# Performance work log

Hardware: AMD Instinct MI355X
Metric: run time of the kernel (lower is better)

The kernel has to match this reference:

```python
import math
import jax, jax.numpy as jnp
import numpy as np

L = 4        # number of base-MLP layers
B = 16       # batch of weight-space samples
N = 256      # base-MLP width (n_in = n_out = N)
C_IN = 16    # input channels per weight entry
C_OUT = 16   # output channels per weight entry
HID = 64     # siren hidden dim
W0 = 1.0
W0_FIRST = 30.0
FINAL_NORM = math.sqrt((2 * L + 7) * C_IN)


def setup_inputs() -> dict:
    key = jax.random.key(0)
    ks = jax.random.split(key, 17)
    d = {}
    for i in range(L):
        d[f"w{i}"] = jax.random.normal(ks[i], (B, N, N, C_IN), jnp.float32) * 0.02
        d[f"b{i}"] = jax.random.normal(ks[L + i], (B, N, C_IN), jnp.float32) * 0.02
    def u(k, shape, scale):
        return jax.random.uniform(k, shape, jnp.float32, -scale, scale)
    # SIREN-style init scales
    d["s_w0"] = u(ks[8], (3, HID), 1.0 / 3.0)
    d["s_b0"] = u(ks[9], (HID,), 1.0 / math.sqrt(3.0))
    d["s_w1"] = u(ks[10], (HID, HID), math.sqrt(6.0 / HID) / W0)
    d["s_b1"] = u(ks[11], (HID,), 1.0 / math.sqrt(HID))
    d["s_w2"] = u(ks[12], (HID, HID), math.sqrt(6.0 / HID) / W0)
    d["s_b2"] = u(ks[13], (HID,), 1.0 / math.sqrt(HID))
    d["s_wo"] = u(ks[14], (HID, C_IN * C_OUT), math.sqrt(6.0 / HID) / W0)
    d["s_bo"] = u(ks[15], (C_IN * C_OUT,), 1.0 / math.sqrt(HID))
    return d


def _siren(x, sp):
    sw0, sb0, sw1, sb1, sw2, sb2, swo, sbo = sp
    h = jnp.sin(W0_FIRST * (x @ sw0 + sb0))
    h = jnp.sin(W0 * (h @ sw1 + sb1))
    h = jnp.sin(W0 * (h @ sw2 + sb2))
    return (h @ swo + sbo) / FINAL_NORM


def _forward(ws, bs, sp):
    term_idx = jnp.linspace(-1.0, 1.0, num=14)
    layer_idx = jnp.linspace(-1.0, 1.0, num=L)
    grid = jnp.stack(jnp.meshgrid(layer_idx, layer_idx, indexing='ij'), axis=-1)  # (L,L,2)

    g_in = jnp.concatenate([jnp.broadcast_to(grid, (4, L, L, 2)),
                            jnp.broadcast_to(term_idx[:4, None, None, None], (4, L, L, 1))], -1)
    global_terms = _siren(g_in, sp).reshape(4, L, L, C_IN, C_OUT)

    dgrid = jnp.transpose(jnp.diagonal(grid))          # (L,2)
    d_in = jnp.concatenate([jnp.broadcast_to(dgrid, (6, L, 2)),
                            jnp.broadcast_to(term_idx[4:10, None, None], (6, L, 1))], -1)
    diag_terms = _siren(d_in, sp).reshape(6, L, C_IN, C_OUT)

    p1 = jnp.transpose(jnp.diagonal(grid, offset=1))   # (L-1,2)
    p1_in = jnp.concatenate([jnp.broadcast_to(p1, (2, L - 1, 2)),
                             jnp.broadcast_to(term_idx[10:12, None, None], (2, L - 1, 1))], -1)
    diag_p1 = _siren(p1_in, sp).reshape(2, L - 1, C_IN, C_OUT)

    m1 = jnp.transpose(jnp.diagonal(grid, offset=-1))  # (L-1,2)
    m1_in = jnp.concatenate([jnp.broadcast_to(m1, (2, L - 1, 2)),
                             jnp.broadcast_to(term_idx[12:14, None, None], (2, L - 1, 1))], -1)
    diag_m1 = _siren(m1_in, sp).reshape(2, L - 1, C_IN, C_OUT)

    t_w_otherw, t_w_otherb = global_terms[0], global_terms[1]
    t_b_otherw, t_b_otherb = global_terms[2], global_terms[3]
    t_w_wrow, t_w_wcol, t_w_w = diag_terms[0], diag_terms[1], diag_terms[2]
    t_w_b, t_b_wcol, t_bb = diag_terms[3], diag_terms[4], diag_terms[5]
    t_w_wm1, t_w_bm1 = diag_m1[0], diag_m1[1]
    t_w_wp1, t_b_wp1 = diag_p1[0], diag_p1[1]

    rsums = [jnp.mean(w, axis=1) for w in ws]          # (B,K,c)
    csums = [jnp.mean(w, axis=2) for w in ws]          # (B,J,c)
    allsums = jnp.stack([jnp.mean(r, axis=1) for r in rsums], -1)  # (B,c,L)
    sums_b = jnp.stack([jnp.mean(b, axis=1) for b in bs], -1)      # (B,c,L)

    outs = []
    for i in range(L):
        ow = jnp.einsum('bjkc,cd->bjkd', ws[i], t_w_w[i])
        ow += jnp.einsum('bcl,lcd->bd', allsums, t_w_otherw[i])[:, None, None, :]
        ow += jnp.einsum('bcl,lcd->bd', sums_b, t_w_otherb[i])[:, None, None, :]
        ow += jnp.einsum('bjc,cd->bjd', csums[i], t_w_wcol[i])[:, :, None, :]
        ow += jnp.einsum('bkc,cd->bkd', rsums[i], t_w_wrow[i])[:, None, :, :]
        ow += jnp.einsum('bkc,cd->bkd', bs[i], t_w_b[i])[:, None, :, :]
        if i > 0:
            ow += jnp.einsum('bjc,cd->bjd', rsums[i - 1], t_w_wm1[i - 1])[:, :, None, :]
            ow += jnp.einsum('bjc,cd->bjd', bs[i - 1], t_w_bm1[i - 1])[:, :, None, :]
        if i < L - 1:
            ow += jnp.einsum('bkc,cd->bkd', csums[i + 1], t_w_wp1[i])[:, None, :, :]
        ob = jnp.einsum('bjc,cd->bjd', bs[i], t_bb[i])
        ob += jnp.einsum('bkc,cd->bkd', rsums[i], t_b_wcol[i])
        if i < L - 1:
            ob += jnp.einsum('bkc,cd->bkd', csums[i + 1], t_b_wp1[i])
        ob += jnp.einsum('bcl,lcd->bd', allsums, t_b_otherw[i])[:, None, :]
        ob += jnp.einsum('bcl,lcd->bd', sums_b, t_b_otherb[i])[:, None, :]
        outs += [ow, ob]
    return tuple(outs)


def reference(w0, w1, w2, w3, b0, b1, b2, b3,
              s_w0, s_b0, s_w1, s_b1, s_w2, s_b2, s_wo, s_bo):
    return _forward([w0, w1, w2, w3], [b0, b1, b2, b3],
                    (s_w0, s_b0, s_w1, s_b1, s_w2, s_b2, s_wo, s_bo))
```

## Files before the change

kernel.cpp:

```cpp
#include <hip/hip_runtime.h>
#include <math.h>

#define DEV_INLINE __device__ __forceinline__

constexpr int Nn = 256;
constexpr size_t SZW = (size_t)16 * 256 * 256 * 16;
constexpr size_t SZB = (size_t)16 * 256 * 16;
constexpr size_t OSTRIDE = SZW + SZB;

constexpr int T_GT = 0;
constexpr int T_DT = 16384;
constexpr int T_P1 = 22528;
constexpr int T_M1 = 24064;
constexpr int O_RS = 25600;
constexpr int O_CS = 287744;
constexpr int O_AS = 549888;
constexpr int O_BS = 550912;
constexpr int O_AROW = 551936;
constexpr int O_BCOL = 814080;

DEV_INLINE void f4acc(float4& a, const float4 b) { a.x += b.x; a.y += b.y; a.z += b.z; a.w += b.w; }
DEV_INLINE float4 f4add(const float4 a, const float4 b) { return make_float4(a.x + b.x, a.y + b.y, a.z + b.z, a.w + b.w); }
DEV_INLINE void f4fma(float4& a, float s, const float4 t) {
    a.x = fmaf(s, t.x, a.x); a.y = fmaf(s, t.y, a.y);
    a.z = fmaf(s, t.z, a.z); a.w = fmaf(s, t.w, a.w);
}

__global__ __launch_bounds__(64) void siren_kernel(
    const float* __restrict__ sw0, const float* __restrict__ sb0,
    const float* __restrict__ sw1, const float* __restrict__ sb1,
    const float* __restrict__ sw2, const float* __restrict__ sb2,
    const float* __restrict__ swo, const float* __restrict__ sbo,
    float* __restrict__ ws) {
    __shared__ float h[64];
    const int p = blockIdx.x, t = threadIdx.x;
    const float lv[4] = {-1.f, -1.f / 3.f, 1.f / 3.f, 1.f};
    float x, y, tt;
    if (p < 64)      { int tm = p >> 4, a = (p >> 2) & 3, bb = p & 3; x = lv[a];   y = lv[bb];  tt = -1.f + 2.f * tm / 13.f; }
    else if (p < 88) { int q = p - 64; int tm = q >> 2, a = q & 3;    x = lv[a];   y = lv[a];   tt = -1.f + 2.f * (4 + tm) / 13.f; }
    else if (p < 94) { int q = p - 88; int tm = q / 3, a = q % 3;     x = lv[a];   y = lv[a+1]; tt = -1.f + 2.f * (10 + tm) / 13.f; }
    else             { int q = p - 94; int tm = q / 3, a = q % 3;     x = lv[a+1]; y = lv[a];   tt = -1.f + 2.f * (12 + tm) / 13.f; }
    float v = sinf(30.f * (x * sw0[t] + y * sw0[64 + t] + tt * sw0[128 + t] + sb0[t]));
    h[t] = v; __syncthreads();
    float v1 = sb1[t];
    for (int u = 0; u < 64; ++u) v1 += h[u] * sw1[u * 64 + t];
    v1 = sinf(v1);
    __syncthreads(); h[t] = v1; __syncthreads();
    float v2 = sb2[t];
    for (int u = 0; u < 64; ++u) v2 += h[u] * sw2[u * 64 + t];
    v2 = sinf(v2);
    __syncthreads(); h[t] = v2; __syncthreads();
    const float inv_fn = 0.06454972243679028f;
    for (int m = 0; m < 4; ++m) {
        int o = m * 64 + t;
        float vo = sbo[o];
        for (int u = 0; u < 64; ++u) vo += h[u] * swo[u * 256 + o];
        ws[p * 256 + o] = vo * inv_fn;
    }
}

__global__ __launch_bounds__(64) void reduce_b_kernel(
    const float4* __restrict__ b0, const float4* __restrict__ b1,
    const float4* __restrict__ b2, const float4* __restrict__ b3,
    float* __restrict__ ws) {
    const int z = blockIdx.x;
    const int l = z >> 4, b = z & 15;
    const float4* bp = ((l == 0) ? b0 : (l == 1) ? b1 : (l == 2) ? b2 : b3) + (size_t)b * Nn * 4;
    const int lane = threadIdx.x;
    const int c4 = lane & 3, part = lane >> 2;
    float4 acc = make_float4(0.f, 0.f, 0.f, 0.f);
    for (int s = 0; s < 16; ++s) f4acc(acc, bp[(size_t)(part + s * 16) * 4 + c4]);
#pragma unroll
    for (int m = 4; m < 64; m <<= 1) {
        acc.x += __shfl_xor(acc.x, m); acc.y += __shfl_xor(acc.y, m);
        acc.z += __shfl_xor(acc.z, m); acc.w += __shfl_xor(acc.w, m);
    }
    if (lane < 4) {
        float* dst = ws + O_BS + (size_t)z * 16 + lane * 4;
        dst[0] = acc.x; dst[1] = acc.y; dst[2] = acc.z; dst[3] = acc.w;
    }
}

__global__ __launch_bounds__(256) void reduce_w_kernel(
    const float4* __restrict__ w0, const float4* __restrict__ w1,
    const float4* __restrict__ w2, const float4* __restrict__ w3,
    float* __restrict__ ws, int bbase) {
    const int kchunk = blockIdx.x, jtile = blockIdx.y, z = blockIdx.z;
    const int l = z >> 2, b = bbase + (z & 3);
    const float4* __restrict__ w = (l == 0) ? w0 : (l == 1) ? w1 : (l == 2) ? w2 : w3;
    const int tid = threadIdx.x;
    const int c4 = tid & 3, jloc = tid >> 2;
    const int j = jtile * 64 + jloc;
    const int lane = tid & 63, wave = tid >> 6;
    __shared__ float4 rpart[4][64][4];
    __shared__ float4 apart[4][4];
    const float4* wrow = w + (size_t)(b * Nn + j) * Nn * 4 + c4;
    const int kbase = kchunk * 64;
    float4 cacc = make_float4(0.f, 0.f, 0.f, 0.f);
#pragma unroll 8
    for (int kk = 0; kk < 64; ++kk) {
        float4 v = wrow[(size_t)(kbase + kk) * 4];
        f4acc(cacc, v);
        float4 r = v;
#pragma unroll
        for (int m = 4; m < 64; m <<= 1) {
            r.x += __shfl_xor(r.x, m); r.y += __shfl_xor(r.y, m);
            r.z += __shfl_xor(r.z, m); r.w += __shfl_xor(r.w, m);
        }
        if (lane < 4) rpart[wave][kk][lane] = r;
    }
    float4 a = cacc;
#pragma unroll
    for (int m = 4; m < 64; m <<= 1) {
        a.x += __shfl_xor(a.x, m); a.y += __shfl_xor(a.y, m);
        a.z += __shfl_xor(a.z, m); a.w += __shfl_xor(a.w, m);
    }
    if (lane < 4) apart[wave][lane] = a;
    __syncthreads();
    float* cdst = ws + O_CS + ((size_t)((l * 16 + b) * Nn + j)) * 16 + c4 * 4;
    atomicAdd(cdst + 0, cacc.x); atomicAdd(cdst + 1, cacc.y);
    atomicAdd(cdst + 2, cacc.z); atomicAdd(cdst + 3, cacc.w);
    const int kk2 = tid >> 2, c42 = tid & 3;
    float4 s = rpart[0][kk2][c42];
    f4acc(s, rpart[1][kk2][c42]); f4acc(s, rpart[2][kk2][c42]); f4acc(s, rpart[3][kk2][c42]);
    float* rdst = ws + O_RS + ((size_t)((l * 16 + b) * Nn + kbase + kk2)) * 16 + c42 * 4;
    atomicAdd(rdst + 0, s.x); atomicAdd(rdst + 1, s.y);
    atomicAdd(rdst + 2, s.z); atomicAdd(rdst + 3, s.w);
    if (tid < 4) {
        float4 s2 = apart[0][tid];
        f4acc(s2, apart[1][tid]); f4acc(s2, apart[2][tid]); f4acc(s2, apart[3][tid]);
        float* adst = ws + O_AS + (size_t)(l * 16 + b) * 16 + tid * 4;
        atomicAdd(adst + 0, s2.x); atomicAdd(adst + 1, s2.y);
        atomicAdd(adst + 2, s2.z); atomicAdd(adst + 3, s2.w);
    }
}

__global__ __launch_bounds__(256) void vectors_kernel(
    const float* __restrict__ bias0, const float* __restrict__ bias1,
    const float* __restrict__ bias2, const float* __restrict__ bias3,
    float* __restrict__ ws, float* __restrict__ out, int bbase) {
    const int g = blockIdx.x * 256 + threadIdx.x;
    const int d = g & 15, n = (g >> 4) & 255, bg = (g >> 12) & 3, l = g >> 14;
    const int b = bbase + bg;
    const float invN = 1.f / 256.f, invNN = 1.f / 65536.f;
    const float* bias[4] = {bias0, bias1, bias2, bias3};
    const size_t rowi = (size_t)((l * 16 + b) * 256 + n) * 16;
    const float* cs = ws + O_CS + rowi;
    const float* rs = ws + O_RS + rowi;
    const float* bv = bias[l] + (size_t)(b * 256 + n) * 16;
    const float* dt = ws + T_DT;
    const float* Twrow  = dt + (0 * 4 + l) * 256;
    const float* Twcol  = dt + (1 * 4 + l) * 256;
    const float* Twb    = dt + (3 * 4 + l) * 256;
    const float* Tbwcol = dt + (4 * 4 + l) * 256;
    const float* Tbb    = dt + (5 * 4 + l) * 256;
    float arow = 0.f, bcol = 0.f, ob = 0.f;
#pragma unroll
    for (int c = 0; c < 16; ++c) {
        float cm = cs[c] * invN, rm = rs[c] * invN, bb = bv[c];
        arow += cm * Twcol[c * 16 + d];
        bcol += rm * Twrow[c * 16 + d] + bb * Twb[c * 16 + d];
        ob   += rm * Tbwcol[c * 16 + d] + bb * Tbb[c * 16 + d];
    }
    if (l > 0) {
        const float* rsm = ws + O_RS + (size_t)(((l - 1) * 16 + b) * 256 + n) * 16;
        const float* bvm = bias[l - 1] + (size_t)(b * 256 + n) * 16;
        const float* Twm1 = ws + T_M1 + (l - 1) * 256;
        const float* Tbm1 = ws + T_M1 + (3 + l - 1) * 256;
#pragma unroll
        for (int c = 0; c < 16; ++c)
            arow += rsm[c] * invN * Twm1[c * 16 + d] + bvm[c] * Tbm1[c * 16 + d];
    }
    if (l < 3) {
        const float* csp = ws + O_CS + (size_t)(((l + 1) * 16 + b) * 256 + n) * 16;
        const float* Twp1  = ws + T_P1 + l * 256;
        const float* Tbwp1 = ws + T_P1 + (3 + l) * 256;
#pragma unroll
        for (int c = 0; c < 16; ++c) {
            float cp = csp[c] * invN;
            bcol += cp * Twp1[c * 16 + d];
            ob   += cp * Tbwp1[c * 16 + d];
        }
    }
#pragma unroll
    for (int ll = 0; ll < 4; ++ll) {
        const float* as_ = ws + O_AS + (size_t)(ll * 16 + b) * 16;
        const float* bs_ = ws + O_BS + (size_t)(ll * 16 + b) * 16;
        const float* g0 = ws + ((0 * 4 + l) * 4 + ll) * 256;
        const float* g1 = ws + ((1 * 4 + l) * 4 + ll) * 256;
        const float* g2 = ws + ((2 * 4 + l) * 4 + ll) * 256;
        const float* g3 = ws + ((3 * 4 + l) * 4 + ll) * 256;
#pragma unroll
        for (int c = 0; c < 16; ++c) {
            float am = as_[c] * invNN, bm = bs_[c] * invN;
            arow += am * g0[c * 16 + d] + bm * g1[c * 16 + d];
            ob   += am * g2[c * 16 + d] + bm * g3[c * 16 + d];
        }
    }
    ws[O_AROW + rowi + d] = arow;
    ws[O_BCOL + rowi + d] = bcol;
    out[(size_t)l * OSTRIDE + SZW + (size_t)(b * 256 + n) * 16 + d] = ob;
}

__global__ __launch_bounds__(256) void transform_kernel(
    const float4* __restrict__ w0, const float4* __restrict__ w1,
    const float4* __restrict__ w2, const float4* __restrict__ w3,
    const float* __restrict__ ws, float4* __restrict__ out, int bbase) {
    const int j = blockIdx.x, bg = blockIdx.y, l = blockIdx.z;
    const int b = bbase + bg;
    const float4* __restrict__ w = (l == 0) ? w0 : (l == 1) ? w1 : (l == 2) ? w2 : w3;
    const int tid = threadIdx.x;
    const int d4 = tid & 3, kk = tid >> 2;
    const float4* T4 = (const float4*)ws + (T_DT / 4) + (2 * 4 + l) * 64;
    float4 t[16];
#pragma unroll
    for (int c = 0; c < 16; ++c) t[c] = T4[c * 4 + d4];
    const size_t rowbase = (size_t)(b * 256 + j) * 256;
    const float4* Ar = (const float4*)(ws + O_AROW);
    const float4* Bc = (const float4*)(ws + O_BCOL) + (size_t)(l * 16 + b) * 256 * 4 + d4;
    const float4 arow = Ar[(size_t)((l * 16 + b) * 256 + j) * 4 + d4];
    const size_t outb = (size_t)l * (OSTRIDE / 4) + rowbase * 4 + d4;
#pragma unroll
    for (int s = 0; s < 4; ++s) {
        const int k = s * 64 + kk;
        float4 acc = f4add(arow, Bc[(size_t)k * 4]);
        const float4* wp = w + (rowbase + k) * 4;
        float4 v0 = wp[0], v1 = wp[1], v2 = wp[2], v3 = wp[3];
        f4fma(acc, v0.x, t[0]);  f4fma(acc, v0.y, t[1]);  f4fma(acc, v0.z, t[2]);  f4fma(acc, v0.w, t[3]);
        f4fma(acc, v1.x, t[4]);  f4fma(acc, v1.y, t[5]);  f4fma(acc, v1.z, t[6]);  f4fma(acc, v1.w, t[7]);
        f4fma(acc, v2.x, t[8]);  f4fma(acc, v2.y, t[9]);  f4fma(acc, v2.z, t[10]); f4fma(acc, v2.w, t[11]);
        f4fma(acc, v3.x, t[12]); f4fma(acc, v3.y, t[13]); f4fma(acc, v3.z, t[14]); f4fma(acc, v3.w, t[15]);
        out[outb + (size_t)k * 4] = acc;
    }
}

extern "C" void kernel_launch(void* const* d_in, const int* in_sizes, int n_in,
                              void* d_out, int out_size, void* d_ws, size_t ws_size,
                              hipStream_t stream) {
    const float *W[4], *Bv[4], *S[8];
    if (in_sizes[1] == in_sizes[0]) {
        for (int i = 0; i < 4; ++i) { W[i] = (const float*)d_in[i]; Bv[i] = (const float*)d_in[4 + i]; }
    } else {
        for (int i = 0; i < 4; ++i) { W[i] = (const float*)d_in[2 * i]; Bv[i] = (const float*)d_in[2 * i + 1]; }
    }
    for (int k = 0; k < 8; ++k) S[k] = (const float*)d_in[8 + k];
    float* ws = (float*)d_ws;
    float* out = (float*)d_out;

    hipMemsetAsync(ws + O_RS, 0, (size_t)(O_AROW - O_RS) * sizeof(float), stream);
    siren_kernel<<<100, 64, 0, stream>>>(S[0], S[1], S[2], S[3], S[4], S[5], S[6], S[7], ws);
    reduce_b_kernel<<<64, 64, 0, stream>>>((const float4*)Bv[0], (const float4*)Bv[1],
                                           (const float4*)Bv[2], (const float4*)Bv[3], ws);
    for (int g = 0; g < 4; ++g) {
        const int bbase = 4 * g;
        reduce_w_kernel<<<dim3(4, 4, 16), 256, 0, stream>>>(
            (const float4*)W[0], (const float4*)W[1], (const float4*)W[2], (const float4*)W[3], ws, bbase);
        vectors_kernel<<<256, 256, 0, stream>>>(Bv[0], Bv[1], Bv[2], Bv[3], ws, out, bbase);
        transform_kernel<<<dim3(256, 4, 4), 256, 0, stream>>>(
            (const float4*)W[0], (const float4*)W[1], (const float4*)W[2], (const float4*)W[3],
            ws, (float4*)out, bbase);
    }
}
```

Measured before the change: 705.4 us.

## Stage 32x32 weight tiles in LDS for row/column sums in reduce_w

```diff
diff --git a/kernel.cpp b/kernel.cpp
--- a/kernel.cpp
+++ b/kernel.cpp
@@ -85,53 +85,64 @@
     const float4* __restrict__ w0, const float4* __restrict__ w1,
     const float4* __restrict__ w2, const float4* __restrict__ w3,
     float* __restrict__ ws, int bbase) {
-    const int kchunk = blockIdx.x, jtile = blockIdx.y, z = blockIdx.z;
-    const int l = z >> 2, b = bbase + (z & 3);
+    const int tile = blockIdx.x;
+    const int kt = tile & 7, jt = tile >> 3;
+    const int lb = blockIdx.y;
+    const int l = lb >> 2, b = bbase + (lb & 3);
     const float4* __restrict__ w = (l == 0) ? w0 : (l == 1) ? w1 : (l == 2) ? w2 : w3;
     const int tid = threadIdx.x;
-    const int c4 = tid & 3, jloc = tid >> 2;
-    const int j = jtile * 64 + jloc;
-    const int lane = tid & 63, wave = tid >> 6;
-    __shared__ float4 rpart[4][64][4];
-    __shared__ float4 apart[4][4];
-    const float4* wrow = w + (size_t)(b * Nn + j) * Nn * 4 + c4;
-    const int kbase = kchunk * 64;
-    float4 cacc = make_float4(0.f, 0.f, 0.f, 0.f);
-#pragma unroll 8
-    for (int kk = 0; kk < 64; ++kk) {
-        float4 v = wrow[(size_t)(kbase + kk) * 4];
-        f4acc(cacc, v);
-        float4 r = v;
-#pragma unroll
-        for (int m = 4; m < 64; m <<= 1) {
-            r.x += __shfl_xor(r.x, m); r.y += __shfl_xor(r.y, m);
-            r.z += __shfl_xor(r.z, m); r.w += __shfl_xor(r.w, m);
-        }
-        if (lane < 4) rpart[wave][kk][lane] = r;
-    }
-    float4 a = cacc;
-#pragma unroll
-    for (int m = 4; m < 64; m <<= 1) {
-        a.x += __shfl_xor(a.x, m); a.y += __shfl_xor(a.y, m);
-        a.z += __shfl_xor(a.z, m); a.w += __shfl_xor(a.w, m);
-    }
-    if (lane < 4) apart[wave][lane] = a;
+
+    __shared__ float4 lds4[4096];
+    __shared__ float asumf[32][16];
+
+    const size_t base = ((size_t)(b * Nn + jt * 32)) * 1024 + (size_t)kt * 128;
+#pragma unroll
+    for (int it = 0; it < 16; ++it) {
+        const int f = it * 256 + tid;
+        const int jl = f >> 7, idx = f & 127;
+        float4 v = w[base + (size_t)jl * 1024 + idx];
+        lds4[jl * 128 + (idx ^ (jl & 7))] = v;
+    }
     __syncthreads();
-    float* cdst = ws + O_CS + ((size_t)((l * 16 + b) * Nn + j)) * 16 + c4 * 4;
-    atomicAdd(cdst + 0, cacc.x); atomicAdd(cdst + 1, cacc.y);
-    atomicAdd(cdst + 2, cacc.z); atomicAdd(cdst + 3, cacc.w);
-    const int kk2 = tid >> 2, c42 = tid & 3;
-    float4 s = rpart[0][kk2][c42];
-    f4acc(s, rpart[1][kk2][c42]); f4acc(s, rpart[2][kk2][c42]); f4acc(s, rpart[3][kk2][c42]);
-    float* rdst = ws + O_RS + ((size_t)((l * 16 + b) * Nn + kbase + kk2)) * 16 + c42 * 4;
-    atomicAdd(rdst + 0, s.x); atomicAdd(rdst + 1, s.y);
-    atomicAdd(rdst + 2, s.z); atomicAdd(rdst + 3, s.w);
-    if (tid < 4) {
-        float4 s2 = apart[0][tid];
-        f4acc(s2, apart[1][tid]); f4acc(s2, apart[2][tid]); f4acc(s2, apart[3][tid]);
-        float* adst = ws + O_AS + (size_t)(l * 16 + b) * 16 + tid * 4;
-        atomicAdd(adst + 0, s2.x); atomicAdd(adst + 1, s2.y);
-        atomicAdd(adst + 2, s2.z); atomicAdd(adst + 3, s2.w);
+
+    const int h = tid & 1, c4 = (tid >> 1) & 3, loc = tid >> 3;
+
+    float4 acc = make_float4(0.f, 0.f, 0.f, 0.f);
+#pragma unroll
+    for (int q = 0; q < 16; ++q) {
+        const int kk = h * 16 + q;
+        f4acc(acc, lds4[loc * 128 + ((kk * 4 + c4) ^ (loc & 7))]);
+    }
+    acc.x += __shfl_xor(acc.x, 1); acc.y += __shfl_xor(acc.y, 1);
+    acc.z += __shfl_xor(acc.z, 1); acc.w += __shfl_xor(acc.w, 1);
+    if (h == 0) {
+        float* cdst = ws + O_CS + ((size_t)((l * 16 + b) * Nn + jt * 32 + loc)) * 16 + c4 * 4;
+        atomicAdd(cdst + 0, acc.x); atomicAdd(cdst + 1, acc.y);
+        atomicAdd(cdst + 2, acc.z); atomicAdd(cdst + 3, acc.w);
+    }
+
+    float4 acc2 = make_float4(0.f, 0.f, 0.f, 0.f);
+#pragma unroll
+    for (int q = 0; q < 16; ++q) {
+        const int jj = h * 16 + q;
+        f4acc(acc2, lds4[jj * 128 + ((loc * 4 + c4) ^ (jj & 7))]);
+    }
+    acc2.x += __shfl_xor(acc2.x, 1); acc2.y += __shfl_xor(acc2.y, 1);
+    acc2.z += __shfl_xor(acc2.z, 1); acc2.w += __shfl_xor(acc2.w, 1);
+    if (h == 0) {
+        float* rdst = ws + O_RS + ((size_t)((l * 16 + b) * Nn + kt * 32 + loc)) * 16 + c4 * 4;
+        atomicAdd(rdst + 0, acc2.x); atomicAdd(rdst + 1, acc2.y);
+        atomicAdd(rdst + 2, acc2.z); atomicAdd(rdst + 3, acc2.w);
+        asumf[loc][c4 * 4 + 0] = acc2.x; asumf[loc][c4 * 4 + 1] = acc2.y;
+        asumf[loc][c4 * 4 + 2] = acc2.z; asumf[loc][c4 * 4 + 3] = acc2.w;
+    }
+    __syncthreads();
+
+    if (tid < 16) {
+        float s = 0.f;
+#pragma unroll
+        for (int kl = 0; kl < 32; ++kl) s += asumf[kl][tid];
+        atomicAdd(ws + O_AS + (size_t)(l * 16 + b) * 16 + tid, s);
     }
 }
 
@@ -253,7 +264,7 @@
                                            (const float4*)Bv[2], (const float4*)Bv[3], ws);
     for (int g = 0; g < 4; ++g) {
         const int bbase = 4 * g;
-        reduce_w_kernel<<<dim3(4, 4, 16), 256, 0, stream>>>(
+        reduce_w_kernel<<<dim3(64, 16), 256, 0, stream>>>(
             (const float4*)W[0], (const float4*)W[1], (const float4*)W[2], (const float4*)W[3], ws, bbase);
         vectors_kernel<<<256, 256, 0, stream>>>(Bv[0], Bv[1], Bv[2], Bv[3], ws, out, bbase);
         transform_kernel<<<dim3(256, 4, 4), 256, 0, stream>>>(
```

New measurement: 644.0 us. -8.7%, faster.
